# Optimization experiments

Hardware: AMD Instinct MI355X
Metric: run time of the kernel (lower is better)

The kernel has to match this reference:

```python
import jax, jax.numpy as jnp
import numpy as np

B, T_HIST, D, H, STEPS = 2048, 15, 64, 128, 20
MAX_STEPS = 48           # max adaptive steps per unit time interval
DT0, RTOL, ATOL = 0.1, 1e-3, 1e-6
SAFETY, FMIN, FMAX = 0.9, 0.2, 10.0

# Tsit5 (Tsitouras 2011) tableau
A21 = 0.161
A31, A32 = -0.008480655492356989, 0.335480655492357
A41, A42, A43 = 2.8971530571054935, -6.359448489975075, 4.3622954328695815
A51, A52, A53, A54 = 5.325864828439257, -11.748883564062828, 7.4955393428898365, -0.09249506636175525
A61, A62, A63, A64, A65 = 5.86145544294642, -12.92096931784711, 8.159367898576159, -0.071584973281401, -0.028269050394068383
B1, B2, B3, B4, B5, B6 = 0.09646076681806523, 0.01, 0.4798896504144996, 1.379008574103742, -3.290069515436081, 2.324710524099774
E1, E2, E3, E4, E5, E6, E7 = (-0.00178001105222577714, -0.0008164344596567469, 0.007880878010261995,
                              -0.1447110071732629, 0.5823571654525552, -0.45808210592918697, 0.015151515151515152)


def _mlp(y, W1, b1, W2, b2, W3, b3):
    h = jax.nn.softplus(y @ W1.T + b1)
    h = jax.nn.softplus(h @ W2.T + b2)
    return h @ W3.T + b3


def _solve(y0, W1, b1, W2, b2, W3, b3, steps):
    f = lambda y: _mlp(y, W1, b1, W2, b2, W3, b3)  # batched vector field [B,D]->[B,D]
    Bn = y0.shape[0]

    def segment(carry, t1):
        y, dt = carry
        t = jnp.full((Bn,), t1 - 1.0, y0.dtype)
        done = jnp.zeros((Bn,), bool)

        def body(state, _):
            t, y, dt, done = state
            dt_c = jnp.minimum(dt, t1 - t)          # clip to segment end
            h = dt_c[:, None]
            k1 = f(y)
            k2 = f(y + h * (A21 * k1))
            k3 = f(y + h * (A31 * k1 + A32 * k2))
            k4 = f(y + h * (A41 * k1 + A42 * k2 + A43 * k3))
            k5 = f(y + h * (A51 * k1 + A52 * k2 + A53 * k3 + A54 * k4))
            k6 = f(y + h * (A61 * k1 + A62 * k2 + A63 * k3 + A64 * k4 + A65 * k5))
            y5 = y + h * (B1 * k1 + B2 * k2 + B3 * k3 + B4 * k4 + B5 * k5 + B6 * k6)
            k7 = f(y5)
            err = h * (E1 * k1 + E2 * k2 + E3 * k3 + E4 * k4 + E5 * k5 + E6 * k6 + E7 * k7)
            scale = ATOL + RTOL * jnp.maximum(jnp.abs(y), jnp.abs(y5))
            err_norm = jnp.sqrt(jnp.mean((err / scale) ** 2, axis=-1))  # [B]
            accept = (err_norm <= 1.0) & (~done)
            factor = jnp.clip(SAFETY * jnp.maximum(err_norm, 1e-10) ** (-0.2), FMIN, FMAX)
            t_new = jnp.where(accept, t + dt_c, t)
            y_new = jnp.where(accept[:, None], y5, y)
            dt_new = jnp.where(done, dt, dt_c * factor)
            done_new = done | (t_new >= t1 - 1e-8)
            return (t_new, y_new, dt_new, done_new), None

        (t, y, dt, done), _ = jax.lax.scan(jax.checkpoint(body), (t, y, dt, done), None, length=MAX_STEPS)
        return (y, dt), y

    ts1 = jnp.arange(1, steps + 1, dtype=y0.dtype)
    dt0 = jnp.full((Bn,), DT0, y0.dtype)
    (_, _), ys = jax.lax.scan(segment, (y0, dt0), ts1)  # ys: [steps, B, D]
    return jnp.transpose(ys, (1, 0, 2))                  # [B, steps, D]


def setup_inputs() -> dict:
    key = jax.random.key(0)
    ks = jax.random.split(key, 7)
    history = jax.random.normal(ks[0], (B, T_HIST, D), jnp.float32)
    # small-scale init keeps the vector field mild so adaptive steps converge
    W1 = jax.random.normal(ks[1], (H, D), jnp.float32) * (0.5 / np.sqrt(D))
    b1 = jax.random.normal(ks[2], (H,), jnp.float32) * 0.05
    W2 = jax.random.normal(ks[3], (H, H), jnp.float32) * (0.5 / np.sqrt(H))
    b2 = jax.random.normal(ks[4], (H,), jnp.float32) * 0.05
    W3 = jax.random.normal(ks[5], (D, H), jnp.float32) * (0.1 / np.sqrt(H))
    b3 = jax.random.normal(ks[6], (D,), jnp.float32) * 0.05
    return {"history": history, "W1": W1, "b1": b1, "W2": W2, "b2": b2, "W3": W3, "b3": b3, "steps": STEPS}


def reference(history, W1, b1, W2, b2, W3, b3, steps):
    y0 = history[:, -1]  # NeuralODE uses only the last history state
    return _solve(y0, W1, b1, W2, b2, W3, b3, steps)
```

## Files before the change

### kernel.cpp

```cpp
#include <hip/hip_runtime.h>
#include <math.h>

#define NB    2048
#define NSEG  20
#define MAXIT 48

typedef __attribute__((ext_vector_type(8))) short bf8_t;
typedef __attribute__((ext_vector_type(4))) float f32x4;

#define cA21 ((float)0.161)
#define cA31 ((float)-0.008480655492356989)
#define cA32 ((float)0.335480655492357)
#define cA41 ((float)2.8971530571054935)
#define cA42 ((float)-6.359448489975075)
#define cA43 ((float)4.3622954328695815)
#define cA51 ((float)5.325864828439257)
#define cA52 ((float)-11.748883564062828)
#define cA53 ((float)7.4955393428898365)
#define cA54 ((float)-0.09249506636175525)
#define cA61 ((float)5.86145544294642)
#define cA62 ((float)-12.92096931784711)
#define cA63 ((float)8.159367898576159)
#define cA64 ((float)-0.071584973281401)
#define cA65 ((float)-0.028269050394068383)
#define cB1  ((float)0.09646076681806523)
#define cB2  ((float)0.01)
#define cB3  ((float)0.4798896504144996)
#define cB4  ((float)1.379008574103742)
#define cB5  ((float)-3.290069515436081)
#define cB6  ((float)2.324710524099774)
#define cE1  ((float)-0.001780011052225777)
#define cE2  ((float)-0.0008164344596567469)
#define cE3  ((float)0.007880878010261995)
#define cE4  ((float)-0.1447110071732629)
#define cE5  ((float)0.5823571654525552)
#define cE6  ((float)-0.45808210592918697)
#define cE7  ((float)0.015151515151515152)

__device__ __forceinline__ void split2(float x, short &hi, short &lo) {
    unsigned u = __float_as_uint(x);
    hi = (short)(u >> 16);
    float r = x - __uint_as_float(u & 0xFFFF0000u);
    lo = (short)(__float_as_uint(r) >> 16);
}

__device__ __forceinline__ float softplus_f(float x) {
    float t = exp2f(-fabsf(x) * 1.442695040888963f);
    return fmaxf(x, 0.0f) + log2f(1.0f + t) * 0.6931471805599453f;
}

__device__ __forceinline__ unsigned pk(short a, short b) {
    return ((unsigned)(unsigned short)a) | (((unsigned)(unsigned short)b) << 16);
}

__global__ __launch_bounds__(512)
void ode_kernel(const float* __restrict__ history,
                const float* __restrict__ W1, const float* __restrict__ b1,
                const float* __restrict__ W2, const float* __restrict__ b2,
                const float* __restrict__ W3, const float* __restrict__ b3,
                float* __restrict__ out)
{
    __shared__ alignas(16) short argH[2 * 544], argL[2 * 544];
    __shared__ alignas(16) short h1H[4 * 544], h1L[4 * 544];
    __shared__ alignas(16) short h2H[4 * 544], h2L[4 * 544];
    __shared__ alignas(16) float kcur[8 * 68];
    __shared__ int doneF[8];

    const int tid  = threadIdx.x;
    const int wave = tid >> 6, lane = tid & 63;
    const int quad = lane >> 4, col = lane & 15;
    const int jb   = 16 * wave + 4 * quad;

    bf8_t A1h[2], A1l[2], A2h[4], A2l[4], A3h[4], A3l[4];
#pragma unroll
    for (int c = 0; c < 2; ++c) {
        const float* p = W1 + (size_t)(16 * wave + col) * 64 + 32 * c + 8 * quad;
        bf8_t h, l;
#pragma unroll
        for (int j = 0; j < 8; ++j) { short hs, ls; split2(p[j], hs, ls); h[j] = hs; l[j] = ls; }
        A1h[c] = h; A1l[c] = l;
    }
#pragma unroll
    for (int c = 0; c < 4; ++c) {
        const float* p = W2 + (size_t)(16 * wave + col) * 128 + 32 * c + 8 * quad;
        bf8_t h, l;
#pragma unroll
        for (int j = 0; j < 8; ++j) { short hs, ls; split2(p[j], hs, ls); h[j] = hs; l[j] = ls; }
        A2h[c] = h; A2l[c] = l;
    }
    f32x4 b3f = {0.f, 0.f, 0.f, 0.f};
    if (wave < 4) {
#pragma unroll
        for (int c = 0; c < 4; ++c) {
            const float* p = W3 + (size_t)(16 * wave + col) * 128 + 32 * c + 8 * quad;
            bf8_t h, l;
#pragma unroll
            for (int j = 0; j < 8; ++j) { short hs, ls; split2(p[j], hs, ls); h[j] = hs; l[j] = ls; }
            A3h[c] = h; A3l[c] = l;
        }
        b3f = *(const f32x4*)(b3 + jb);
    } else {
        bf8_t z = {0, 0, 0, 0, 0, 0, 0, 0};
#pragma unroll
        for (int c = 0; c < 4; ++c) { A3h[c] = z; A3l[c] = z; }
    }
    const f32x4 b1f = *(const f32x4*)(b1 + jb);
    const f32x4 b2f = *(const f32x4*)(b2 + jb);

    const int aidx = (lane >> 5) * 544 + ((lane >> 3) & 3) * 136 + wave * 8 + (lane & 7);
    const int elem = blockIdx.x * 8 + wave;

    auto gemm = [&](const bf8_t* Ah, const bf8_t* Al, const short* BH, const short* BL,
                    int nch) -> f32x4 {
        f32x4 acc = {0.f, 0.f, 0.f, 0.f};
#pragma unroll
        for (int c = 0; c < nch; ++c) {
            const int off = c * 544 + quad * 136 + col * 8;
            bf8_t bh = *(const bf8_t*)(BH + off);
            bf8_t bl = *(const bf8_t*)(BL + off);
            acc = __builtin_amdgcn_mfma_f32_16x16x32_bf16(Al[c], bh, acc, 0, 0, 0);
            acc = __builtin_amdgcn_mfma_f32_16x16x32_bf16(Ah[c], bl, acc, 0, 0, 0);
            acc = __builtin_amdgcn_mfma_f32_16x16x32_bf16(Ah[c], bh, acc, 0, 0, 0);
        }
        return acc;
    };

    auto epi = [&](f32x4 acc, f32x4 bias, short* H, short* L) {
        if (col < 8) {
            const int idx = (jb >> 5) * 544 + ((jb >> 3) & 3) * 136 + col * 8 + (jb & 7);
            short hh[4], ll[4];
#pragma unroll
            for (int r = 0; r < 4; ++r) {
                float v = softplus_f(acc[r] + bias[r]);
                split2(v, hh[r], ll[r]);
            }
            *(uint2*)(H + idx) = make_uint2(pk(hh[0], hh[1]), pk(hh[2], hh[3]));
            *(uint2*)(L + idx) = make_uint2(pk(ll[0], ll[1]), pk(ll[2], ll[3]));
        }
    };

    auto eval = [&]() {
        __syncthreads();
        f32x4 a1 = gemm(A1h, A1l, argH, argL, 2);
        epi(a1, b1f, h1H, h1L);
        __syncthreads();
        f32x4 a2 = gemm(A2h, A2l, h1H, h1L, 4);
        epi(a2, b2f, h2H, h2L);
        __syncthreads();
        if (wave < 4) {
            f32x4 a3 = gemm(A3h, A3l, h2H, h2L, 4);
            if (col < 8) {
                f32x4 kv;
#pragma unroll
                for (int r = 0; r < 4; ++r) kv[r] = a3[r] + b3f[r];
                *(f32x4*)(kcur + col * 68 + jb) = kv;
            }
        }
        __syncthreads();
    };

    float y  = history[((size_t)elem * 15 + 14) * 64 + lane];
    float dt = 0.1f;
    float k1, k2, k3, k4, k5, k6;

    {
        short hi, lo; split2(y, hi, lo);
        argH[aidx] = hi; argL[aidx] = lo;
        eval();
        k1 = kcur[wave * 68 + lane];
    }

#pragma unroll 1
    for (int seg = 1; seg <= NSEG; ++seg) {
        const float t1 = (float)seg;
        float t = t1 - 1.0f;
        bool done = false;

#pragma unroll 1
        for (int it = 0; it < MAXIT; ++it) {
            const float dt_c = fminf(dt, t1 - t);
            const float h = dt_c;
            float y5v = 0.f, k7v = 0.f;

#pragma unroll 1
            for (int st = 2; st <= 7; ++st) {
                float sum;
                switch (st) {
                    case 2: sum = cA21 * k1; break;
                    case 3: sum = fmaf(cA31, k1, cA32 * k2); break;
                    case 4: sum = fmaf(cA41, k1, fmaf(cA42, k2, cA43 * k3)); break;
                    case 5: sum = fmaf(cA51, k1, fmaf(cA52, k2, fmaf(cA53, k3, cA54 * k4))); break;
                    case 6: sum = fmaf(cA61, k1, fmaf(cA62, k2, fmaf(cA63, k3, fmaf(cA64, k4, cA65 * k5)))); break;
                    default: sum = fmaf(cB1, k1, fmaf(cB2, k2, fmaf(cB3, k3, fmaf(cB4, k4, fmaf(cB5, k5, cB6 * k6))))); break;
                }
                float arg = fmaf(h, sum, y);
                if (st == 7) y5v = arg;
                short hi, lo; split2(arg, hi, lo);
                argH[aidx] = hi; argL[aidx] = lo;
                eval();
                float kv = kcur[wave * 68 + lane];
                switch (st) {
                    case 2: k2 = kv; break;
                    case 3: k3 = kv; break;
                    case 4: k4 = kv; break;
                    case 5: k5 = kv; break;
                    case 6: k6 = kv; break;
                    default: k7v = kv; break;
                }
            }

            float esum = fmaf(cE1, k1, fmaf(cE2, k2, fmaf(cE3, k3,
                         fmaf(cE4, k4, fmaf(cE5, k5, fmaf(cE6, k6, cE7 * k7v))))));
            float err = h * esum;
            float sc = fmaf(1e-3f, fmaxf(fabsf(y), fabsf(y5v)), 1e-6f);
            float r = err / sc;
            float rr = r * r;
#pragma unroll
            for (int off = 32; off > 0; off >>= 1) rr += __shfl_xor(rr, off, 64);
            float en = sqrtf(rr * (1.0f / 64.0f));

            bool accept = (en <= 1.0f) && !done;
            float fac = 0.9f * exp2f(-0.2f * log2f(fmaxf(en, 1e-10f)));
            fac = fminf(fmaxf(fac, 0.2f), 10.0f);

            if (accept) { t += dt_c; y = y5v; k1 = k7v; }
            if (!done) dt = dt_c * fac;
            done = done || (t >= t1 - 1e-8f);

            if (lane == 0) doneF[wave] = done ? 1 : 0;
            __syncthreads();
            bool all = true;
#pragma unroll
            for (int e2 = 0; e2 < 8; ++e2) all = all && (doneF[e2] != 0);
            if (all) break;
        }

        out[((size_t)elem * NSEG + (seg - 1)) * 64 + lane] = y;
    }
}

extern "C" void kernel_launch(void* const* d_in, const int* in_sizes, int n_in,
                              void* d_out, int out_size, void* d_ws, size_t ws_size,
                              hipStream_t stream) {
    const float* history = (const float*)d_in[0];
    const float* W1 = (const float*)d_in[1];
    const float* b1 = (const float*)d_in[2];
    const float* W2 = (const float*)d_in[3];
    const float* b2 = (const float*)d_in[4];
    const float* W3 = (const float*)d_in[5];
    const float* b3 = (const float*)d_in[6];
    float* out = (float*)d_out;

    ode_kernel<<<dim3(NB / 8), dim3(512), 0, stream>>>(history, W1, b1, W2, b2, W3, b3, out);
}
```

Before: 335.7 us.

## Keep ODE state in MFMA output layout and fold hi/lo split into the K dimension

The solver state and stage derivatives now live in registers in the MFMA accumulator layout, so the k-vector no longer round-trips through shared memory and the final barrier of each MLP evaluation is removed. The bf16 hi/lo operands are interleaved into one buffer along K, which cuts each chunk from three MFMAs to two. The missing cross term is recovered with a lane shuffle. Error-norm reduction uses shared partial sums, and the done-check uses __syncthreads_and. This reshuffles which lanes hold which elements and drops one precision term (the Al*Bl product, already absent before), so accuracy is close to the old path but the numerics are subtly different.

```diff
diff --git a/kernel.cpp b/kernel.cpp
--- a/kernel.cpp
+++ b/kernel.cpp
@@ -53,6 +53,8 @@
     return ((unsigned)(unsigned short)a) | (((unsigned)(unsigned short)b) << 16);
 }
 
+__device__ __forceinline__ float sx8(float v) { return __shfl_xor(v, 8, 64); }
+
 __global__ __launch_bounds__(512)
 void ode_kernel(const float* __restrict__ history,
                 const float* __restrict__ W1, const float* __restrict__ b1,
@@ -60,16 +62,17 @@
                 const float* __restrict__ W3, const float* __restrict__ b3,
                 float* __restrict__ out)
 {
-    __shared__ alignas(16) short argH[2 * 544], argL[2 * 544];
-    __shared__ alignas(16) short h1H[4 * 544], h1L[4 * 544];
-    __shared__ alignas(16) short h2H[4 * 544], h2L[4 * 544];
-    __shared__ alignas(16) float kcur[8 * 68];
-    __shared__ int doneF[8];
+    __shared__ alignas(16) short argC[2 * 544];
+    __shared__ alignas(16) short h1C[4 * 544];
+    __shared__ alignas(16) short h2C[4 * 544];
+    __shared__ float partS[32];
 
     const int tid  = threadIdx.x;
     const int wave = tid >> 6, lane = tid & 63;
     const int quad = lane >> 4, col = lane & 15;
     const int jb   = 16 * wave + 4 * quad;
+    const bool w03  = (wave < 4);
+    const bool real = w03 && (col < 8);
 
     bf8_t A1h[2], A1l[2], A2h[4], A2l[4], A3h[4], A3l[4];
 #pragma unroll
@@ -89,7 +92,7 @@
         A2h[c] = h; A2l[c] = l;
     }
     f32x4 b3f = {0.f, 0.f, 0.f, 0.f};
-    if (wave < 4) {
+    if (w03) {
 #pragma unroll
         for (int c = 0; c < 4; ++c) {
             const float* p = W3 + (size_t)(16 * wave + col) * 128 + 32 * c + 8 * quad;
@@ -107,135 +110,154 @@
     const f32x4 b1f = *(const f32x4*)(b1 + jb);
     const f32x4 b2f = *(const f32x4*)(b2 + jb);
 
-    const int aidx = (lane >> 5) * 544 + ((lane >> 3) & 3) * 136 + wave * 8 + (lane & 7);
-    const int elem = blockIdx.x * 8 + wave;
-
-    auto gemm = [&](const bf8_t* Ah, const bf8_t* Al, const short* BH, const short* BL,
-                    int nch) -> f32x4 {
-        f32x4 acc = {0.f, 0.f, 0.f, 0.f};
-#pragma unroll
+    const int wIdx = (jb >> 5) * 544 + ((jb >> 3) & 3) * 136 + (jb & 7);
+
+    auto gemm2 = [&](const bf8_t* Ah, const bf8_t* Al, const short* B, int nch) -> f32x4 {
+        bf8_t bf[4];
+#pragma unroll 4
+        for (int c = 0; c < nch; ++c)
+            bf[c] = *(const bf8_t*)(B + c * 544 + quad * 136 + col * 8);
+        f32x4 d1 = {0.f, 0.f, 0.f, 0.f}, d2 = {0.f, 0.f, 0.f, 0.f};
+#pragma unroll 4
         for (int c = 0; c < nch; ++c) {
-            const int off = c * 544 + quad * 136 + col * 8;
-            bf8_t bh = *(const bf8_t*)(BH + off);
-            bf8_t bl = *(const bf8_t*)(BL + off);
-            acc = __builtin_amdgcn_mfma_f32_16x16x32_bf16(Al[c], bh, acc, 0, 0, 0);
-            acc = __builtin_amdgcn_mfma_f32_16x16x32_bf16(Ah[c], bl, acc, 0, 0, 0);
-            acc = __builtin_amdgcn_mfma_f32_16x16x32_bf16(Ah[c], bh, acc, 0, 0, 0);
-        }
-        return acc;
-    };
-
-    auto epi = [&](f32x4 acc, f32x4 bias, short* H, short* L) {
+            d1 = __builtin_amdgcn_mfma_f32_16x16x32_bf16(Ah[c], bf[c], d1, 0, 0, 0);
+            d2 = __builtin_amdgcn_mfma_f32_16x16x32_bf16(Al[c], bf[c], d2, 0, 0, 0);
+        }
+        f32x4 o;
+#pragma unroll
+        for (int r = 0; r < 4; ++r) o[r] = d1[r] + sx8(d1[r]) + d2[r];
+        return o;
+    };
+
+    auto epiwr = [&](f32x4 pre, f32x4 bias, short* H) {
         if (col < 8) {
-            const int idx = (jb >> 5) * 544 + ((jb >> 3) & 3) * 136 + col * 8 + (jb & 7);
             short hh[4], ll[4];
 #pragma unroll
             for (int r = 0; r < 4; ++r) {
-                float v = softplus_f(acc[r] + bias[r]);
+                float v = softplus_f(pre[r] + bias[r]);
                 split2(v, hh[r], ll[r]);
             }
-            *(uint2*)(H + idx) = make_uint2(pk(hh[0], hh[1]), pk(hh[2], hh[3]));
-            *(uint2*)(L + idx) = make_uint2(pk(ll[0], ll[1]), pk(ll[2], ll[3]));
-        }
-    };
-
-    auto eval = [&]() {
+            *(uint2*)(H + wIdx + col * 8)       = make_uint2(pk(hh[0], hh[1]), pk(hh[2], hh[3]));
+            *(uint2*)(H + wIdx + (col + 8) * 8) = make_uint2(pk(ll[0], ll[1]), pk(ll[2], ll[3]));
+        }
+    };
+
+    auto writeArg = [&](f32x4 a) {
+        if (real) {
+            short hh[4], ll[4];
+#pragma unroll
+            for (int r = 0; r < 4; ++r) split2(a[r], hh[r], ll[r]);
+            *(uint2*)(argC + wIdx + col * 8)       = make_uint2(pk(hh[0], hh[1]), pk(hh[2], hh[3]));
+            *(uint2*)(argC + wIdx + (col + 8) * 8) = make_uint2(pk(ll[0], ll[1]), pk(ll[2], ll[3]));
+        }
+    };
+
+    auto evalK = [&]() -> f32x4 {
         __syncthreads();
-        f32x4 a1 = gemm(A1h, A1l, argH, argL, 2);
-        epi(a1, b1f, h1H, h1L);
+        f32x4 p1 = gemm2(A1h, A1l, argC, 2);
+        epiwr(p1, b1f, h1C);
         __syncthreads();
-        f32x4 a2 = gemm(A2h, A2l, h1H, h1L, 4);
-        epi(a2, b2f, h2H, h2L);
+        f32x4 p2 = gemm2(A2h, A2l, h1C, 4);
+        epiwr(p2, b2f, h2C);
         __syncthreads();
-        if (wave < 4) {
-            f32x4 a3 = gemm(A3h, A3l, h2H, h2L, 4);
-            if (col < 8) {
-                f32x4 kv;
-#pragma unroll
-                for (int r = 0; r < 4; ++r) kv[r] = a3[r] + b3f[r];
-                *(f32x4*)(kcur + col * 68 + jb) = kv;
-            }
-        }
-        __syncthreads();
-    };
-
-    float y  = history[((size_t)elem * 15 + 14) * 64 + lane];
+        f32x4 kv = {0.f, 0.f, 0.f, 0.f};
+        if (w03) {
+            f32x4 p3 = gemm2(A3h, A3l, h2C, 4);
+#pragma unroll
+            for (int r = 0; r < 4; ++r) kv[r] = p3[r] + b3f[r];
+        }
+        return kv;
+    };
+
+    const int eb = blockIdx.x * 8;
+    f32x4 y = {0.f, 0.f, 0.f, 0.f};
+    if (real)
+        y = *(const f32x4*)(history + ((size_t)(eb + col) * 15 + 14) * 64 + jb);
     float dt = 0.1f;
-    float k1, k2, k3, k4, k5, k6;
-
-    {
-        short hi, lo; split2(y, hi, lo);
-        argH[aidx] = hi; argL[aidx] = lo;
-        eval();
-        k1 = kcur[wave * 68 + lane];
-    }
+    float t = 0.f;
+    f32x4 k1, k2, k3, k4, k5, k6;
+
+    writeArg(y);
+    k1 = evalK();
 
 #pragma unroll 1
     for (int seg = 1; seg <= NSEG; ++seg) {
         const float t1 = (float)seg;
-        float t = t1 - 1.0f;
+        t = t1 - 1.0f;
         bool done = false;
 
 #pragma unroll 1
         for (int it = 0; it < MAXIT; ++it) {
             const float dt_c = fminf(dt, t1 - t);
             const float h = dt_c;
-            float y5v = 0.f, k7v = 0.f;
+            f32x4 y5 = {0.f, 0.f, 0.f, 0.f}, k7 = {0.f, 0.f, 0.f, 0.f};
 
 #pragma unroll 1
             for (int st = 2; st <= 7; ++st) {
-                float sum;
-                switch (st) {
-                    case 2: sum = cA21 * k1; break;
-                    case 3: sum = fmaf(cA31, k1, cA32 * k2); break;
-                    case 4: sum = fmaf(cA41, k1, fmaf(cA42, k2, cA43 * k3)); break;
-                    case 5: sum = fmaf(cA51, k1, fmaf(cA52, k2, fmaf(cA53, k3, cA54 * k4))); break;
-                    case 6: sum = fmaf(cA61, k1, fmaf(cA62, k2, fmaf(cA63, k3, fmaf(cA64, k4, cA65 * k5)))); break;
-                    default: sum = fmaf(cB1, k1, fmaf(cB2, k2, fmaf(cB3, k3, fmaf(cB4, k4, fmaf(cB5, k5, cB6 * k6))))); break;
+                f32x4 a;
+#pragma unroll
+                for (int r = 0; r < 4; ++r) {
+                    float sum;
+                    switch (st) {
+                        case 2: sum = cA21 * k1[r]; break;
+                        case 3: sum = fmaf(cA31, k1[r], cA32 * k2[r]); break;
+                        case 4: sum = fmaf(cA41, k1[r], fmaf(cA42, k2[r], cA43 * k3[r])); break;
+                        case 5: sum = fmaf(cA51, k1[r], fmaf(cA52, k2[r], fmaf(cA53, k3[r], cA54 * k4[r]))); break;
+                        case 6: sum = fmaf(cA61, k1[r], fmaf(cA62, k2[r], fmaf(cA63, k3[r], fmaf(cA64, k4[r], cA65 * k5[r])))); break;
+                        default: sum = fmaf(cB1, k1[r], fmaf(cB2, k2[r], fmaf(cB3, k3[r], fmaf(cB4, k4[r], fmaf(cB5, k5[r], cB6 * k6[r]))))); break;
+                    }
+                    a[r] = fmaf(h, sum, y[r]);
                 }
-                float arg = fmaf(h, sum, y);
-                if (st == 7) y5v = arg;
-                short hi, lo; split2(arg, hi, lo);
-                argH[aidx] = hi; argL[aidx] = lo;
-                eval();
-                float kv = kcur[wave * 68 + lane];
+                if (st == 7) y5 = a;
+                writeArg(a);
+                f32x4 kv = evalK();
                 switch (st) {
                     case 2: k2 = kv; break;
                     case 3: k3 = kv; break;
                     case 4: k4 = kv; break;
                     case 5: k5 = kv; break;
                     case 6: k6 = kv; break;
-                    default: k7v = kv; break;
+                    default: k7 = kv; break;
                 }
             }
 
-            float esum = fmaf(cE1, k1, fmaf(cE2, k2, fmaf(cE3, k3,
-                         fmaf(cE4, k4, fmaf(cE5, k5, fmaf(cE6, k6, cE7 * k7v))))));
-            float err = h * esum;
-            float sc = fmaf(1e-3f, fmaxf(fabsf(y), fabsf(y5v)), 1e-6f);
-            float r = err / sc;
-            float rr = r * r;
-#pragma unroll
-            for (int off = 32; off > 0; off >>= 1) rr += __shfl_xor(rr, off, 64);
-            float en = sqrtf(rr * (1.0f / 64.0f));
-
+            float rr = 0.f;
+            if (real) {
+#pragma unroll
+                for (int r = 0; r < 4; ++r) {
+                    float es = fmaf(cE1, k1[r], fmaf(cE2, k2[r], fmaf(cE3, k3[r],
+                               fmaf(cE4, k4[r], fmaf(cE5, k5[r], fmaf(cE6, k6[r], cE7 * k7[r]))))));
+                    float e = h * es;
+                    float sc = fmaf(1e-3f, fmaxf(fabsf(y[r]), fabsf(y5[r])), 1e-6f);
+                    float q = e / sc;
+                    rr = fmaf(q, q, rr);
+                }
+            }
+            rr += __shfl_xor(rr, 16, 64);
+            rr += __shfl_xor(rr, 32, 64);
+            if (real && quad == 0) partS[wave * 8 + col] = rr;
+            __syncthreads();
+
+            float en = 0.f;
+            if (w03) {
+                int cc = col & 7;
+                en = sqrtf((partS[cc] + partS[8 + cc] + partS[16 + cc] + partS[24 + cc])
+                           * (1.0f / 64.0f));
+            }
             bool accept = (en <= 1.0f) && !done;
             float fac = 0.9f * exp2f(-0.2f * log2f(fmaxf(en, 1e-10f)));
             fac = fminf(fmaxf(fac, 0.2f), 10.0f);
 
-            if (accept) { t += dt_c; y = y5v; k1 = k7v; }
+            if (accept) { t += dt_c; y = y5; k1 = k7; }
             if (!done) dt = dt_c * fac;
             done = done || (t >= t1 - 1e-8f);
 
-            if (lane == 0) doneF[wave] = done ? 1 : 0;
-            __syncthreads();
-            bool all = true;
-#pragma unroll
-            for (int e2 = 0; e2 < 8; ++e2) all = all && (doneF[e2] != 0);
-            if (all) break;
-        }
-
-        out[((size_t)elem * NSEG + (seg - 1)) * 64 + lane] = y;
+            int my = real ? (done ? 1 : 0) : 1;
+            if (__syncthreads_and(my)) break;
+        }
+
+        if (real)
+            *(f32x4*)(out + ((size_t)(eb + col) * NSEG + (seg - 1)) * 64 + jb) = y;
     }
 }
 
```

New measurement: 384.5 us. +14.6%, slower.

## Drop low-half split of hidden activations and use independent MFMA accumulators

Applied to the files above, without the earlier changes.

Hidden activations are now stored as a single round-to-nearest bf16 instead of a hi/lo pair. This removes the low-part shared-memory traffic and one of the three MFMAs per chunk in layers 2 and 3. The GEMMs load all B fragments first and accumulate into three independent accumulators, which breaks the serial MFMA dependency chain. The per-wave done flag array plus barrier is replaced with __syncthreads_and. Precision falls to about bf16 on the hidden activations, which could alter how many adaptive steps are accepted and the accuracy margin.

```diff
diff --git a/kernel.cpp b/kernel.cpp
--- a/kernel.cpp
+++ b/kernel.cpp
@@ -5,8 +5,8 @@
 #define NSEG  20
 #define MAXIT 48
 
-typedef __attribute__((ext_vector_type(8))) short bf8_t;
-typedef __attribute__((ext_vector_type(4))) float f32x4;
+typedef short bf8_t __attribute__((ext_vector_type(8)));
+typedef float f32x4 __attribute__((ext_vector_type(4)));
 
 #define cA21 ((float)0.161)
 #define cA31 ((float)-0.008480655492356989)
@@ -44,6 +44,11 @@
     lo = (short)(__float_as_uint(r) >> 16);
 }
 
+__device__ __forceinline__ short bf16rne(float x) {
+    unsigned u = __float_as_uint(x);
+    return (short)((u + 0x7FFFu + ((u >> 16) & 1u)) >> 16);
+}
+
 __device__ __forceinline__ float softplus_f(float x) {
     float t = exp2f(-fabsf(x) * 1.442695040888963f);
     return fmaxf(x, 0.0f) + log2f(1.0f + t) * 0.6931471805599453f;
@@ -61,15 +66,15 @@
                 float* __restrict__ out)
 {
     __shared__ alignas(16) short argH[2 * 544], argL[2 * 544];
-    __shared__ alignas(16) short h1H[4 * 544], h1L[4 * 544];
-    __shared__ alignas(16) short h2H[4 * 544], h2L[4 * 544];
+    __shared__ alignas(16) short h1H[4 * 544];
+    __shared__ alignas(16) short h2H[4 * 544];
     __shared__ alignas(16) float kcur[8 * 68];
-    __shared__ int doneF[8];
 
     const int tid  = threadIdx.x;
     const int wave = tid >> 6, lane = tid & 63;
     const int quad = lane >> 4, col = lane & 15;
     const int jb   = 16 * wave + 4 * quad;
+    const bool w03 = (wave < 4);
 
     bf8_t A1h[2], A1l[2], A2h[4], A2l[4], A3h[4], A3l[4];
 #pragma unroll
@@ -89,7 +94,7 @@
         A2h[c] = h; A2l[c] = l;
     }
     f32x4 b3f = {0.f, 0.f, 0.f, 0.f};
-    if (wave < 4) {
+    if (w03) {
 #pragma unroll
         for (int c = 0; c < 4; ++c) {
             const float* p = W3 + (size_t)(16 * wave + col) * 128 + 32 * c + 8 * quad;
@@ -99,65 +104,83 @@
             A3h[c] = h; A3l[c] = l;
         }
         b3f = *(const f32x4*)(b3 + jb);
-    } else {
-        bf8_t z = {0, 0, 0, 0, 0, 0, 0, 0};
-#pragma unroll
-        for (int c = 0; c < 4; ++c) { A3h[c] = z; A3l[c] = z; }
     }
     const f32x4 b1f = *(const f32x4*)(b1 + jb);
     const f32x4 b2f = *(const f32x4*)(b2 + jb);
 
-    const int aidx = (lane >> 5) * 544 + ((lane >> 3) & 3) * 136 + wave * 8 + (lane & 7);
-    const int elem = blockIdx.x * 8 + wave;
-
-    auto gemm = [&](const bf8_t* Ah, const bf8_t* Al, const short* BH, const short* BL,
-                    int nch) -> f32x4 {
-        f32x4 acc = {0.f, 0.f, 0.f, 0.f};
-#pragma unroll
+    const int wIdx = (jb >> 5) * 544 + ((jb >> 3) & 3) * 136 + (jb & 7);
+
+    auto gemm3 = [&](const bf8_t* Ah, const bf8_t* Al,
+                     const short* BH, const short* BL, int nch) -> f32x4 {
+        bf8_t bh[4], bl[4];
+#pragma unroll 4
         for (int c = 0; c < nch; ++c) {
             const int off = c * 544 + quad * 136 + col * 8;
-            bf8_t bh = *(const bf8_t*)(BH + off);
-            bf8_t bl = *(const bf8_t*)(BL + off);
-            acc = __builtin_amdgcn_mfma_f32_16x16x32_bf16(Al[c], bh, acc, 0, 0, 0);
-            acc = __builtin_amdgcn_mfma_f32_16x16x32_bf16(Ah[c], bl, acc, 0, 0, 0);
-            acc = __builtin_amdgcn_mfma_f32_16x16x32_bf16(Ah[c], bh, acc, 0, 0, 0);
-        }
-        return acc;
-    };
-
-    auto epi = [&](f32x4 acc, f32x4 bias, short* H, short* L) {
+            bh[c] = *(const bf8_t*)(BH + off);
+            bl[c] = *(const bf8_t*)(BL + off);
+        }
+        f32x4 p1 = {0.f, 0.f, 0.f, 0.f}, p2 = {0.f, 0.f, 0.f, 0.f}, p3 = {0.f, 0.f, 0.f, 0.f};
+#pragma unroll 4
+        for (int c = 0; c < nch; ++c) {
+            p1 = __builtin_amdgcn_mfma_f32_16x16x32_bf16(Al[c], bh[c], p1, 0, 0, 0);
+            p2 = __builtin_amdgcn_mfma_f32_16x16x32_bf16(Ah[c], bl[c], p2, 0, 0, 0);
+            p3 = __builtin_amdgcn_mfma_f32_16x16x32_bf16(Ah[c], bh[c], p3, 0, 0, 0);
+        }
+        f32x4 o;
+#pragma unroll
+        for (int r = 0; r < 4; ++r) o[r] = (p1[r] + p2[r]) + p3[r];
+        return o;
+    };
+
+    auto gemm2 = [&](const bf8_t* Ah, const bf8_t* Al, const short* BH, int nch) -> f32x4 {
+        bf8_t bh[4];
+#pragma unroll 4
+        for (int c = 0; c < nch; ++c)
+            bh[c] = *(const bf8_t*)(BH + c * 544 + quad * 136 + col * 8);
+        f32x4 p1 = {0.f, 0.f, 0.f, 0.f}, p3 = {0.f, 0.f, 0.f, 0.f};
+#pragma unroll 4
+        for (int c = 0; c < nch; ++c) {
+            p1 = __builtin_amdgcn_mfma_f32_16x16x32_bf16(Al[c], bh[c], p1, 0, 0, 0);
+            p3 = __builtin_amdgcn_mfma_f32_16x16x32_bf16(Ah[c], bh[c], p3, 0, 0, 0);
+        }
+        f32x4 o;
+#pragma unroll
+        for (int r = 0; r < 4; ++r) o[r] = p1[r] + p3[r];
+        return o;
+    };
+
+    auto epiH = [&](f32x4 pre, f32x4 bias, short* H) {
         if (col < 8) {
-            const int idx = (jb >> 5) * 544 + ((jb >> 3) & 3) * 136 + col * 8 + (jb & 7);
-            short hh[4], ll[4];
-#pragma unroll
-            for (int r = 0; r < 4; ++r) {
-                float v = softplus_f(acc[r] + bias[r]);
-                split2(v, hh[r], ll[r]);
-            }
-            *(uint2*)(H + idx) = make_uint2(pk(hh[0], hh[1]), pk(hh[2], hh[3]));
-            *(uint2*)(L + idx) = make_uint2(pk(ll[0], ll[1]), pk(ll[2], ll[3]));
+            short hh[4];
+#pragma unroll
+            for (int r = 0; r < 4; ++r)
+                hh[r] = bf16rne(softplus_f(pre[r] + bias[r]));
+            *(uint2*)(H + wIdx + col * 8) = make_uint2(pk(hh[0], hh[1]), pk(hh[2], hh[3]));
         }
     };
 
     auto eval = [&]() {
         __syncthreads();
-        f32x4 a1 = gemm(A1h, A1l, argH, argL, 2);
-        epi(a1, b1f, h1H, h1L);
-        __syncthreads();
-        f32x4 a2 = gemm(A2h, A2l, h1H, h1L, 4);
-        epi(a2, b2f, h2H, h2L);
-        __syncthreads();
-        if (wave < 4) {
-            f32x4 a3 = gemm(A3h, A3l, h2H, h2L, 4);
+        f32x4 q1 = gemm3(A1h, A1l, argH, argL, 2);
+        epiH(q1, b1f, h1H);
+        __syncthreads();
+        f32x4 q2 = gemm2(A2h, A2l, h1H, 4);
+        epiH(q2, b2f, h2H);
+        __syncthreads();
+        if (w03) {
+            f32x4 q3 = gemm2(A3h, A3l, h2H, 4);
             if (col < 8) {
                 f32x4 kv;
 #pragma unroll
-                for (int r = 0; r < 4; ++r) kv[r] = a3[r] + b3f[r];
+                for (int r = 0; r < 4; ++r) kv[r] = q3[r] + b3f[r];
                 *(f32x4*)(kcur + col * 68 + jb) = kv;
             }
         }
         __syncthreads();
     };
+
+    const int elem = blockIdx.x * 8 + wave;
+    const int aidx = (lane >> 5) * 544 + ((lane >> 3) & 3) * 136 + wave * 8 + (lane & 7);
 
     float y  = history[((size_t)elem * 15 + 14) * 64 + lane];
     float dt = 0.1f;
@@ -227,12 +250,7 @@
             if (!done) dt = dt_c * fac;
             done = done || (t >= t1 - 1e-8f);
 
-            if (lane == 0) doneF[wave] = done ? 1 : 0;
-            __syncthreads();
-            bool all = true;
-#pragma unroll
-            for (int e2 = 0; e2 < 8; ++e2) all = all && (doneF[e2] != 0);
-            if (all) break;
+            if (__syncthreads_and(done ? 1 : 0)) break;
         }
 
         out[((size_t)elem * NSEG + (seg - 1)) * 64 + lane] = y;
```

Result: slower. 981.5 us (+192.4%).
